# Performance work log

Hardware: AMD Instinct MI355X
Metric: run time of the kernel (lower is better)

The kernel has to match this reference:

```python
import jax, jax.numpy as jnp
import numpy as np

N, DV, M, DC = 1024, 4, 512, 8
E = N * DV  # 4096 edges; N*DV == M*DC
EPS32 = jnp.float32(1.1920929e-07)  # torch.finfo(torch.float32).eps


def _build_masks():
    rng = np.random.default_rng(0)
    var_of_edge = np.repeat(np.arange(N), DV)                # edge -> variable node
    chk_of_edge = rng.permutation(np.repeat(np.arange(M), DC))  # edge -> check node
    eye = np.eye(E, dtype=bool)
    w_in_to_odd = np.zeros((N, E), dtype=np.float32)
    w_in_to_odd[var_of_edge, np.arange(E)] = 1.0
    same_var = var_of_edge[:, None] == var_of_edge[None, :]
    same_chk = chk_of_edge[:, None] == chk_of_edge[None, :]
    w_even_to_odd = (same_var & ~eye).astype(np.float32)     # extrinsic var-node connectivity
    w_odd_to_even = (same_chk & ~eye).astype(np.float32)     # extrinsic check-node connectivity
    w_even_to_out = np.zeros((E, N), dtype=np.float32)
    w_even_to_out[np.arange(E), var_of_edge] = 1.0
    return w_in_to_odd, w_odd_to_even, w_even_to_odd, w_even_to_out


def setup_inputs() -> dict:
    key = jax.random.key(0)
    w_in_to_odd, w_odd_to_even, w_even_to_odd, w_even_to_out = _build_masks()
    x = 2.0 * jax.random.normal(key, (N, 1), dtype=jnp.float32)  # channel LLRs
    return {
        "x": x,
        "w_in_to_odd": jnp.asarray(w_in_to_odd),
        "w_odd_to_even": jnp.asarray(w_odd_to_even),
        "w_even_to_odd": jnp.asarray(w_even_to_odd),
        "w_even_to_out": jnp.asarray(w_even_to_out),
    }


def _activation_even(odd, w_odd_to_even):
    # odd: [E,1]; repeat across columns then mask -> aux[i,j] = w[i,j]*odd[i]
    aux = w_odd_to_even * odd                      # [E,E]
    aux = jnp.where(aux == 0.0, 1.0, aux)          # zeros (non-edges) -> multiplicative identity
    v = jnp.prod(aux, axis=0)                      # [E] product over incoming messages
    v = jnp.where(v >= 1.0, 1.0 - EPS32, v)
    v = jnp.where(v <= -1.0, -1.0 + EPS32, v)
    return (2.0 * jnp.arctanh(v))[:, None]         # [E,1]


def reference(x, w_in_to_odd, w_odd_to_even, w_even_to_odd, w_even_to_out):
    llr_part = w_in_to_odd.T @ x                   # [E,1], reused every odd layer
    # layer 1: even input is zeros (first_even_layer_output / first_w_even_to_odd)
    odd = jnp.tanh(0.5 * llr_part)
    even = _activation_even(odd, w_odd_to_even)
    for _ in range(4):                             # iterations 2..5 (shared 'rnn'/'spa' weights)
        odd = jnp.tanh(0.5 * (llr_part + w_even_to_odd.T @ even))
        even = _activation_even(odd, w_odd_to_even)
    out = x + w_even_to_out.T @ even               # [N,1]
    return jax.nn.sigmoid(out)
```

## Files before the change

### kernel.cpp

```cpp
#include <hip/hip_runtime.h>


#define En 4096
#define Nn 1024
#define Mn 512
#define EPSF 1.1920929e-07f

__global__ __launch_bounds__(256) void find_first_peer(
    const float* __restrict__ w, int* __restrict__ f) {
  const int lane = threadIdx.x & 63;
  const int wv   = threadIdx.x >> 6;
  const int row  = blockIdx.x * 4 + wv;
  const float4* rowp = (const float4*)(w + (size_t)row * En);

  for (int base = 0; base < En; base += 256) {
    float4 v = rowp[(base >> 2) + lane];
    bool any = (v.x != 0.0f) | (v.y != 0.0f) | (v.z != 0.0f) | (v.w != 0.0f);
    unsigned long long m = __ballot(any);
    if (m) {
      if (lane == __ffsll((unsigned long long)m) - 1) {
        int off = (v.x != 0.0f) ? 0 : (v.y != 0.0f) ? 1 : (v.z != 0.0f) ? 2 : 3;
        f[row] = base + 4 * lane + off;
      }
      break;
    }
  }
}

__global__ __launch_bounds__(1024) void solve(
    const float* __restrict__ x, const int* __restrict__ f_g,
    float* __restrict__ out) {
  __shared__ int   fs[En];
  __shared__ int   slotmap[En];
  __shared__ int   ce[En];
  __shared__ float ods[En];
  __shared__ float evs[En];
  __shared__ int   cnt[Mn];
  __shared__ int   nchk;
  const int t = threadIdx.x;

#pragma unroll
  for (int k = 0; k < 4; ++k) fs[t + k * 1024] = f_g[t + k * 1024];
  if (t < Mn) cnt[t] = 0;
  if (t == 0) nchk = 0;
  __syncthreads();

  int keys[4];
#pragma unroll
  for (int k = 0; k < 4; ++k) {
    int e   = 4 * t + k;
    int fe  = fs[e];
    int ffe = fs[fe];
    int key = (ffe == e && e < fe) ? e : fe;
    keys[k] = key;
    if (key == e) slotmap[e] = atomicAdd(&nchk, 1);
  }
  __syncthreads();
#pragma unroll
  for (int k = 0; k < 4; ++k) {
    int e = 4 * t + k;
    int c = slotmap[keys[k]];
    int p = atomicAdd(&cnt[c], 1);
    ce[c * 8 + p] = e;
  }
  __syncthreads();
  if (t < Mn) {
    int v[8];
#pragma unroll
    for (int k = 0; k < 8; ++k) v[k] = ce[t * 8 + k];
    for (int i = 1; i < 8; ++i) {
      int key = v[i], j = i - 1;
      for (; j >= 0 && v[j] > key; --j) v[j + 1] = v[j];
      v[j + 1] = key;
    }
#pragma unroll
    for (int k = 0; k < 8; ++k) ce[t * 8 + k] = v[k];
  }

  const float xt  = x[t];
  const float th0 = tanhf(0.5f * xt);
#pragma unroll
  for (int k = 0; k < 4; ++k) ods[4 * t + k] = th0;
  __syncthreads();

  for (int it = 0; it < 5; ++it) {
    if (t < Mn) {
      int e[8];
      float f[8];
#pragma unroll
      for (int k = 0; k < 8; ++k) e[k] = ce[t * 8 + k];
#pragma unroll
      for (int k = 0; k < 8; ++k) {
        float o = ods[e[k]];
        f[k] = (o == 0.0f) ? 1.0f : o;
      }
#pragma unroll
      for (int k = 0; k < 8; ++k) {
        float v = 1.0f;
#pragma unroll
        for (int j = 0; j < 8; ++j)
          if (j != k) v *= f[j];
        if (v >= 1.0f)       v =  1.0f - EPSF;
        else if (v <= -1.0f) v = -1.0f + EPSF;
        evs[e[k]] = 2.0f * atanhf(v);
      }
    }
    __syncthreads();

    if (it < 4) {
      float ev[4];
#pragma unroll
      for (int k = 0; k < 4; ++k) ev[k] = evs[4 * t + k];
#pragma unroll
      for (int k = 0; k < 4; ++k) {
        float s = 0.0f;
#pragma unroll
        for (int j = 0; j < 4; ++j)
          if (j != k) s += ev[j];
        ods[4 * t + k] = tanhf(0.5f * (xt + s));
      }
      __syncthreads();
    }
  }

  float s4 = evs[4 * t] + evs[4 * t + 1] + evs[4 * t + 2] + evs[4 * t + 3];
  float z  = xt + s4;
  out[t]   = 1.0f / (1.0f + expf(-z));
}

extern "C" void kernel_launch(void* const* d_in, const int* in_sizes, int n_in,
                              void* d_out, int out_size, void* d_ws,
                              size_t ws_size, hipStream_t stream) {
  const float* x    = (const float*)d_in[0];
  const float* w_oe = (const float*)d_in[2];
  float* out = (float*)d_out;

  int* f = (int*)d_ws;

  find_first_peer<<<dim3(1024), dim3(256), 0, stream>>>(w_oe, f);
  solve<<<dim3(1), dim3(1024), 0, stream>>>(x, f, out);
}
```

Baseline: 170.3 us.

## Prefetch mask rows, use ballot-based slot assignment and split check-node work across threads

The peer-finding kernel now keeps three row chunks in flight so the early-exit scan is not bound by one load per step. The single-block solver replaces the serialized atomic slot counter with a wave ballot prefix scan, and swaps insertion sort for a sorting network. It uses vectorized shared-memory accesses and spreads each check node's eight extrinsic products over two threads with a prefix/suffix style product, so all 1024 threads work in the check phase. Each thread now loads all eight messages, which duplicates some shared reads and arithmetic.

After: 173.5 us. About the same (+1.9%).

```diff
diff --git a/kernel.cpp b/kernel.cpp
--- a/kernel.cpp
+++ b/kernel.cpp
@@ -13,17 +13,24 @@
   const int row  = blockIdx.x * 4 + wv;
   const float4* rowp = (const float4*)(w + (size_t)row * En);
 
-  for (int base = 0; base < En; base += 256) {
-    float4 v = rowp[(base >> 2) + lane];
-    bool any = (v.x != 0.0f) | (v.y != 0.0f) | (v.z != 0.0f) | (v.w != 0.0f);
+  float4 v0 = rowp[lane];
+  float4 v1 = rowp[64 + lane];
+  float4 v2 = rowp[128 + lane];
+  for (int base = 0;; base += 256) {
+    bool any = (v0.x != 0.0f) | (v0.y != 0.0f) | (v0.z != 0.0f) | (v0.w != 0.0f);
     unsigned long long m = __ballot(any);
     if (m) {
-      if (lane == __ffsll((unsigned long long)m) - 1) {
-        int off = (v.x != 0.0f) ? 0 : (v.y != 0.0f) ? 1 : (v.z != 0.0f) ? 2 : 3;
+      if (lane == __ffsll(m) - 1) {
+        int off = (v0.x != 0.0f) ? 0 : (v0.y != 0.0f) ? 1 : (v0.z != 0.0f) ? 2 : 3;
         f[row] = base + 4 * lane + off;
       }
       break;
     }
+    v0 = v1;
+    v1 = v2;
+    int nxt = base + 768;
+    if (nxt > En - 256) nxt = En - 256;
+    v2 = rowp[(nxt >> 2) + lane];
   }
 }
 
@@ -36,96 +43,129 @@
   __shared__ float ods[En];
   __shared__ float evs[En];
   __shared__ int   cnt[Mn];
-  __shared__ int   nchk;
-  const int t = threadIdx.x;
+  __shared__ int   wtot[16];
+  const int t    = threadIdx.x;
+  const int lane = t & 63;
+  const int wv   = t >> 6;
 
-#pragma unroll
-  for (int k = 0; k < 4; ++k) fs[t + k * 1024] = f_g[t + k * 1024];
+  int4 fv = ((const int4*)f_g)[t];
+  *((int4*)&fs[4 * t]) = fv;
   if (t < Mn) cnt[t] = 0;
-  if (t == 0) nchk = 0;
   __syncthreads();
 
-  int keys[4];
+  const int fearr[4] = {fv.x, fv.y, fv.z, fv.w};
+  int  keys[4];
+  bool ismin[4];
 #pragma unroll
   for (int k = 0; k < 4; ++k) {
     int e   = 4 * t + k;
-    int fe  = fs[e];
+    int fe  = fearr[k];
     int ffe = fs[fe];
-    int key = (ffe == e && e < fe) ? e : fe;
-    keys[k] = key;
-    if (key == e) slotmap[e] = atomicAdd(&nchk, 1);
+    keys[k]  = (ffe == e && e < fe) ? e : fe;
+    ismin[k] = (keys[k] == e);
+  }
+  const unsigned long long ltmask = (1ull << lane) - 1ull;
+  int pre = 0;
+  int rank[4];
+#pragma unroll
+  for (int k = 0; k < 4; ++k) {
+    unsigned long long b = __ballot(ismin[k]);
+    rank[k] = pre + (int)__popcll(b & ltmask);
+    pre    += (int)__popcll(b);
+  }
+  if (lane == 0) wtot[wv] = pre;
+  __syncthreads();
+  int wbase = 0;
+  for (int w = 0; w < wv; ++w) wbase += wtot[w];
+#pragma unroll
+  for (int k = 0; k < 4; ++k)
+    if (ismin[k]) slotmap[4 * t + k] = wbase + rank[k];
+  __syncthreads();
+
+#pragma unroll
+  for (int k = 0; k < 4; ++k) {
+    int c = slotmap[keys[k]];
+    int p = atomicAdd(&cnt[c], 1);
+    ce[c * 8 + p] = 4 * t + k;
+  }
+  const float xt  = x[t];
+  const float th0 = tanhf(0.5f * xt);
+  *((float4*)&ods[4 * t]) = make_float4(th0, th0, th0, th0);
+  __syncthreads();
+
+  if (t < Mn) {
+    int4 a = *((int4*)&ce[t * 8]);
+    int4 b = *((int4*)&ce[t * 8 + 4]);
+    int s0 = a.x, s1 = a.y, s2 = a.z, s3 = a.w;
+    int s4 = b.x, s5 = b.y, s6 = b.z, s7 = b.w;
+#define CEX(p, q) { int lo_ = min(p, q), hi_ = max(p, q); p = lo_; q = hi_; }
+    CEX(s0, s1); CEX(s2, s3); CEX(s0, s2); CEX(s1, s3); CEX(s1, s2);
+    CEX(s4, s5); CEX(s6, s7); CEX(s4, s6); CEX(s5, s7); CEX(s5, s6);
+    CEX(s0, s4); CEX(s2, s6); CEX(s1, s5); CEX(s3, s7);
+    CEX(s2, s4); CEX(s3, s5);
+    CEX(s1, s2); CEX(s3, s4); CEX(s5, s6);
+#undef CEX
+    *((int4*)&ce[t * 8])     = make_int4(s0, s1, s2, s3);
+    *((int4*)&ce[t * 8 + 4]) = make_int4(s4, s5, s6, s7);
   }
   __syncthreads();
+
+  const int c = t >> 1;
+  const int h = t & 1;
+  int e[8];
 #pragma unroll
-  for (int k = 0; k < 4; ++k) {
-    int e = 4 * t + k;
-    int c = slotmap[keys[k]];
-    int p = atomicAdd(&cnt[c], 1);
-    ce[c * 8 + p] = e;
-  }
-  __syncthreads();
-  if (t < Mn) {
-    int v[8];
+  for (int k = 0; k < 8; ++k) e[k] = ce[c * 8 + k];
+  int eo[4];
 #pragma unroll
-    for (int k = 0; k < 8; ++k) v[k] = ce[t * 8 + k];
-    for (int i = 1; i < 8; ++i) {
-      int key = v[i], j = i - 1;
-      for (; j >= 0 && v[j] > key; --j) v[j + 1] = v[j];
-      v[j + 1] = key;
+  for (int kk = 0; kk < 4; ++kk) eo[kk] = h ? e[4 + kk] : e[kk];
+
+  for (int it = 0; it < 5; ++it) {
+    float f[8];
+#pragma unroll
+    for (int k = 0; k < 8; ++k) {
+      float o = ods[e[k]];
+      f[k] = (o == 0.0f) ? 1.0f : o;
+    }
+    float v[8];
+    float p = 1.0f;
+#pragma unroll
+    for (int k = 0; k < 8; ++k) {
+      float vv = p;
+#pragma unroll
+      for (int j = k + 1; j < 8; ++j) vv *= f[j];
+      v[k] = vv;
+      p *= f[k];
     }
 #pragma unroll
-    for (int k = 0; k < 8; ++k) ce[t * 8 + k] = v[k];
-  }
-
-  const float xt  = x[t];
-  const float th0 = tanhf(0.5f * xt);
-#pragma unroll
-  for (int k = 0; k < 4; ++k) ods[4 * t + k] = th0;
-  __syncthreads();
-
-  for (int it = 0; it < 5; ++it) {
-    if (t < Mn) {
-      int e[8];
-      float f[8];
-#pragma unroll
-      for (int k = 0; k < 8; ++k) e[k] = ce[t * 8 + k];
-#pragma unroll
-      for (int k = 0; k < 8; ++k) {
-        float o = ods[e[k]];
-        f[k] = (o == 0.0f) ? 1.0f : o;
-      }
-#pragma unroll
-      for (int k = 0; k < 8; ++k) {
-        float v = 1.0f;
-#pragma unroll
-        for (int j = 0; j < 8; ++j)
-          if (j != k) v *= f[j];
-        if (v >= 1.0f)       v =  1.0f - EPSF;
-        else if (v <= -1.0f) v = -1.0f + EPSF;
-        evs[e[k]] = 2.0f * atanhf(v);
-      }
+    for (int kk = 0; kk < 4; ++kk) {
+      float vv = h ? v[4 + kk] : v[kk];
+      if (vv >= 1.0f)       vv =  1.0f - EPSF;
+      else if (vv <= -1.0f) vv = -1.0f + EPSF;
+      evs[eo[kk]] = 2.0f * atanhf(vv);
     }
     __syncthreads();
 
     if (it < 4) {
-      float ev[4];
-#pragma unroll
-      for (int k = 0; k < 4; ++k) ev[k] = evs[4 * t + k];
+      float4 e4 = *((const float4*)&evs[4 * t]);
+      float ev[4] = {e4.x, e4.y, e4.z, e4.w};
+      float od[4];
 #pragma unroll
       for (int k = 0; k < 4; ++k) {
         float s = 0.0f;
 #pragma unroll
         for (int j = 0; j < 4; ++j)
           if (j != k) s += ev[j];
-        ods[4 * t + k] = tanhf(0.5f * (xt + s));
+        od[k] = tanhf(0.5f * (xt + s));
       }
+      *((float4*)&ods[4 * t]) = make_float4(od[0], od[1], od[2], od[3]);
       __syncthreads();
     }
   }
 
-  float s4 = evs[4 * t] + evs[4 * t + 1] + evs[4 * t + 2] + evs[4 * t + 3];
-  float z  = xt + s4;
-  out[t]   = 1.0f / (1.0f + expf(-z));
+  float4 e4 = *((const float4*)&evs[4 * t]);
+  float s4  = e4.x + e4.y + e4.z + e4.w;
+  float z   = xt + s4;
+  out[t]    = 1.0f / (1.0f + expf(-z));
 }
 
 extern "C" void kernel_launch(void* const* d_in, const int* in_sizes, int n_in,
```
